# Performance work log

Measured on AMD Instinct MI355X. Metric: run time of the kernel, lower is better.

The kernel has to match this reference:

```python
import jax, jax.numpy as jnp
import numpy as np

B, C = 2097152, 15   # batch, num_category (15 hardcoded in original via sum_term/15)
EPS = 1e-32
ALPHA = 0.1


def setup_inputs() -> dict:
    key = jax.random.key(0)
    k1, k2 = jax.random.split(key)
    output = jax.random.normal(k1, (B, C), dtype=jnp.float32)
    labels = jax.random.randint(k2, (B, C), 0, 2).astype(jnp.float32)  # 0/1 targets
    return {"output": output, "labels": labels}


def reference(output, labels):
    # outs_sig = sigmoid(output[:, :C])
    sig = jax.nn.sigmoid(output)                      # [B, C]

    # Per-category AUC-hinge penalty. The original builds the full
    # num_pos x num_neg outer-difference matrix and takes its mean, which
    # equals 1 - mean(pos) + mean(neg); empty sides contribute 0 (matching
    # the num_pos==0 / num_neg==0 branches where trans_* = 0).
    pos = labels                                      # 1 where label==1
    neg = 1.0 - labels                                # 1 where label==0
    npos = jnp.sum(pos, axis=0)                       # [C]
    nneg = jnp.sum(neg, axis=0)                       # [C]
    mean_pos = jnp.where(npos > 0, jnp.sum(sig * pos, axis=0) / jnp.maximum(npos, 1.0), 0.0)
    mean_neg = jnp.where(nneg > 0, jnp.sum(sig * neg, axis=0) / jnp.maximum(nneg, 1.0), 0.0)
    penalty = 1.0 - mean_pos + mean_neg               # [C]
    sum_term = jnp.sum(penalty)

    # CEL: applies sigmoid AGAIN to outs_sig (faithful to original double sigmoid)
    s2 = jax.nn.sigmoid(sig)
    cel = (-jnp.mean(labels * jnp.log(s2 + EPS))
           - jnp.mean((1.0 - labels) * jnp.log(1.0 - s2 + EPS)))

    cls = cel + ALPHA * (sum_term / 15.0)
    return (cls, ALPHA * penalty[-1])
```

## Files before the change

kernel.cpp:

```cpp
#include <hip/hip_runtime.h>


#define CATS 15
#define NBLOCKS 960
#define NTHREADS 256

__global__ __launch_bounds__(NTHREADS) void mauch_main(
    const float* __restrict__ outp, const float* __restrict__ labp,
    float* __restrict__ ws, int nFloat4)
{
    const int t = blockIdx.x * blockDim.x + threadIdx.x;
    const int stride = gridDim.x * blockDim.x;

    float ssig[4]  = {0.f, 0.f, 0.f, 0.f};
    float spos[4]  = {0.f, 0.f, 0.f, 0.f};
    float snp[4]   = {0.f, 0.f, 0.f, 0.f};
    float cel = 0.f;

    const float4* o4 = (const float4*)outp;
    const float4* l4 = (const float4*)labp;

    for (int f = t; f < nFloat4; f += stride) {
        float4 ov = o4[f];
        float4 lv = l4[f];
#pragma unroll
        for (int j = 0; j < 4; ++j) {
            float x = (&ov.x)[j];
            float l = (&lv.x)[j];
            float e   = __expf(-x);
            float sig = __builtin_amdgcn_rcpf(1.0f + e);
            float sp  = __logf(1.0f + __expf(-sig));
            ssig[j] += sig;
            spos[j] += sig * l;
            snp[j]  += l;
            cel     += sp + (1.0f - l) * sig;
        }
    }

    __shared__ float red[3 * CATS + 1];
    for (int i = threadIdx.x; i < 3 * CATS + 1; i += blockDim.x) red[i] = 0.f;
    __syncthreads();

    int base = (4 * t) % CATS;
#pragma unroll
    for (int j = 0; j < 4; ++j) {
        int c = base + j; if (c >= CATS) c -= CATS;
        atomicAdd(&red[c],            ssig[j]);
        atomicAdd(&red[CATS + c],     spos[j]);
        atomicAdd(&red[2 * CATS + c], snp[j]);
    }
    atomicAdd(&red[3 * CATS], cel);
    __syncthreads();

    for (int i = threadIdx.x; i < 3 * CATS + 1; i += blockDim.x)
        atomicAdd(&ws[i], red[i]);
}

__global__ void mauch_final(const float* __restrict__ ws, float* __restrict__ out,
                            float invBC, float rowsB)
{
    if (threadIdx.x == 0 && blockIdx.x == 0) {
        float sum_term = 0.f, pen_last = 0.f;
#pragma unroll
        for (int c = 0; c < CATS; ++c) {
            float ssig = ws[c];
            float sp   = ws[CATS + c];
            float np   = ws[2 * CATS + c];
            float nn   = rowsB - np;
            float sneg = ssig - sp;
            float mp = (np > 0.f) ? sp   / fmaxf(np, 1.f) : 0.f;
            float mn = (nn > 0.f) ? sneg / fmaxf(nn, 1.f) : 0.f;
            float pen = 1.f - mp + mn;
            sum_term += pen;
            if (c == CATS - 1) pen_last = pen;
        }
        float cel = ws[3 * CATS] * invBC;
        out[0] = cel + 0.1f * (sum_term / 15.f);
        out[1] = 0.1f * pen_last;
    }
}

extern "C" void kernel_launch(void* const* d_in, const int* in_sizes, int n_in,
                              void* d_out, int out_size, void* d_ws, size_t ws_size,
                              hipStream_t stream) {
    const float* outp = (const float*)d_in[0];
    const float* labp = (const float*)d_in[1];
    float* out = (float*)d_out;
    float* ws  = (float*)d_ws;

    const int total   = in_sizes[0];
    const int nFloat4 = total / 4;
    const float rowsB = (float)(total / CATS);
    const float invBC = 1.0f / (float)total;

    hipMemsetAsync(ws, 0, (3 * CATS + 1) * sizeof(float), stream);

    mauch_main<<<NBLOCKS, NTHREADS, 0, stream>>>(outp, labp, ws, nFloat4);
    mauch_final<<<1, 64, 0, stream>>>(ws, out, invBC, rowsB);
}
```

Measured before the change: 276.1 us.

## Fuse finalize into main kernel via last-block counter and prefetch loads

Removes the separate finalize kernel by having the last block to finish (tracked by an atomic counter in the workspace) compute the final outputs. It also doubles the grid size and software-pipelines the grid-stride loop so the next float4 pair loads while the current one is processed. This saves one kernel launch and aims to hide memory latency, at the cost of a threadfence and counter atomic per block and more global atomics.

Correctness check on the category mapping: a float4 index f = t + i*stride covers category base (4f) % 15. With 1920*256 threads, stride*4 is a multiple of 15, so (4f) % 15 equals (4t) % 15 as the code assumes. That also holds for the tail element.

```diff
diff --git a/kernel.cpp b/kernel.cpp
--- a/kernel.cpp
+++ b/kernel.cpp
@@ -2,43 +2,64 @@
 
 
 #define CATS 15
-#define NBLOCKS 960
+#define NBLOCKS 1920
 #define NTHREADS 256
+#define NSUMS (3 * CATS + 1)
+
+__device__ __forceinline__ void accum_elem(float x, float l,
+                                           float& ssig, float& spos, float& snp,
+                                           float& cel) {
+    float e   = __expf(-x);
+    float sig = __builtin_amdgcn_rcpf(1.0f + e);
+    float sp  = __logf(1.0f + __expf(-sig));
+    ssig += sig;
+    spos += sig * l;
+    snp  += l;
+    cel  += sp + (1.0f - l) * sig;
+}
 
 __global__ __launch_bounds__(NTHREADS) void mauch_main(
     const float* __restrict__ outp, const float* __restrict__ labp,
-    float* __restrict__ ws, int nFloat4)
+    float* __restrict__ ws, float* __restrict__ out,
+    int nFloat4, float invBC, float rowsB)
 {
     const int t = blockIdx.x * blockDim.x + threadIdx.x;
     const int stride = gridDim.x * blockDim.x;
 
-    float ssig[4]  = {0.f, 0.f, 0.f, 0.f};
-    float spos[4]  = {0.f, 0.f, 0.f, 0.f};
-    float snp[4]   = {0.f, 0.f, 0.f, 0.f};
+    float ssig[4] = {0.f, 0.f, 0.f, 0.f};
+    float spos[4] = {0.f, 0.f, 0.f, 0.f};
+    float snp[4]  = {0.f, 0.f, 0.f, 0.f};
     float cel = 0.f;
 
     const float4* o4 = (const float4*)outp;
     const float4* l4 = (const float4*)labp;
 
-    for (int f = t; f < nFloat4; f += stride) {
-        float4 ov = o4[f];
-        float4 lv = l4[f];
+    const int iters = nFloat4 / stride;
+
+    float4 ov = o4[t];
+    float4 lv = l4[t];
+    for (int i = 1; i <= iters; ++i) {
+        float4 co = ov, cl = lv;
+        if (i < iters) {
+            int fn = t + i * stride;
+            ov = o4[fn];
+            lv = l4[fn];
+        }
 #pragma unroll
-        for (int j = 0; j < 4; ++j) {
-            float x = (&ov.x)[j];
-            float l = (&lv.x)[j];
-            float e   = __expf(-x);
-            float sig = __builtin_amdgcn_rcpf(1.0f + e);
-            float sp  = __logf(1.0f + __expf(-sig));
-            ssig[j] += sig;
-            spos[j] += sig * l;
-            snp[j]  += l;
-            cel     += sp + (1.0f - l) * sig;
-        }
+        for (int j = 0; j < 4; ++j)
+            accum_elem((&co.x)[j], (&cl.x)[j], ssig[j], spos[j], snp[j], cel);
+    }
+    int ft = t + iters * stride;
+    if (ft < nFloat4) {
+        float4 co = o4[ft];
+        float4 cl = l4[ft];
+#pragma unroll
+        for (int j = 0; j < 4; ++j)
+            accum_elem((&co.x)[j], (&cl.x)[j], ssig[j], spos[j], snp[j], cel);
     }
 
-    __shared__ float red[3 * CATS + 1];
-    for (int i = threadIdx.x; i < 3 * CATS + 1; i += blockDim.x) red[i] = 0.f;
+    __shared__ float red[NSUMS];
+    for (int i = threadIdx.x; i < NSUMS; i += blockDim.x) red[i] = 0.f;
     __syncthreads();
 
     int base = (4 * t) % CATS;
@@ -52,31 +73,38 @@
     atomicAdd(&red[3 * CATS], cel);
     __syncthreads();
 
-    for (int i = threadIdx.x; i < 3 * CATS + 1; i += blockDim.x)
-        atomicAdd(&ws[i], red[i]);
-}
+    if (threadIdx.x < NSUMS) atomicAdd(&ws[threadIdx.x], red[threadIdx.x]);
+    __threadfence();
+    __syncthreads();
 
-__global__ void mauch_final(const float* __restrict__ ws, float* __restrict__ out,
-                            float invBC, float rowsB)
-{
-    if (threadIdx.x == 0 && blockIdx.x == 0) {
-        float sum_term = 0.f, pen_last = 0.f;
+    __shared__ int isLast;
+    if (threadIdx.x == 0) {
+        unsigned int* ctr = (unsigned int*)(ws + NSUMS);
+        isLast = (atomicAdd(ctr, 1u) == (unsigned int)(gridDim.x - 1));
+    }
+    __syncthreads();
+    if (isLast) {
+        if (threadIdx.x < NSUMS) red[threadIdx.x] = atomicAdd(&ws[threadIdx.x], 0.0f);
+        __syncthreads();
+        if (threadIdx.x == 0) {
+            float sum_term = 0.f, pen_last = 0.f;
 #pragma unroll
-        for (int c = 0; c < CATS; ++c) {
-            float ssig = ws[c];
-            float sp   = ws[CATS + c];
-            float np   = ws[2 * CATS + c];
-            float nn   = rowsB - np;
-            float sneg = ssig - sp;
-            float mp = (np > 0.f) ? sp   / fmaxf(np, 1.f) : 0.f;
-            float mn = (nn > 0.f) ? sneg / fmaxf(nn, 1.f) : 0.f;
-            float pen = 1.f - mp + mn;
-            sum_term += pen;
-            if (c == CATS - 1) pen_last = pen;
+            for (int c = 0; c < CATS; ++c) {
+                float s   = red[c];
+                float sp  = red[CATS + c];
+                float np  = red[2 * CATS + c];
+                float nn  = rowsB - np;
+                float sneg = s - sp;
+                float mp = (np > 0.f) ? sp   / fmaxf(np, 1.f) : 0.f;
+                float mn = (nn > 0.f) ? sneg / fmaxf(nn, 1.f) : 0.f;
+                float pen = 1.f - mp + mn;
+                sum_term += pen;
+                if (c == CATS - 1) pen_last = pen;
+            }
+            float celv = red[3 * CATS] * invBC;
+            out[0] = celv + 0.1f * (sum_term / 15.f);
+            out[1] = 0.1f * pen_last;
         }
-        float cel = ws[3 * CATS] * invBC;
-        out[0] = cel + 0.1f * (sum_term / 15.f);
-        out[1] = 0.1f * pen_last;
     }
 }
 
@@ -93,8 +121,8 @@
     const float rowsB = (float)(total / CATS);
     const float invBC = 1.0f / (float)total;
 
-    hipMemsetAsync(ws, 0, (3 * CATS + 1) * sizeof(float), stream);
+    hipMemsetAsync(ws, 0, (NSUMS + 1) * sizeof(float), stream);
 
-    mauch_main<<<NBLOCKS, NTHREADS, 0, stream>>>(outp, labp, ws, nFloat4);
-    mauch_final<<<1, 64, 0, stream>>>(ws, out, invBC, rowsB);
+    mauch_main<<<NBLOCKS, NTHREADS, 0, stream>>>(outp, labp, ws, out,
+                                                 nFloat4, invBC, rowsB);
 }
```

Result: slower. 443.0 us (+60.4%).
